# Optimization experiments

Measured on AMD Instinct MI355X. Metric: run time of the kernel, lower is better.

## Reference

```python
import jax, jax.numpy as jnp
import numpy as np

LABEL_SIZE = 64
START = LABEL_SIZE - 2
STOP = LABEL_SIZE - 1
NEG = -10000.0


def setup_inputs() -> dict:
    key = jax.random.key(0)
    k1, k2 = jax.random.split(key)
    B, T, L = 512, 512, LABEL_SIZE
    emissions = jax.random.normal(k1, (B, T, L), dtype=jnp.float32)
    # xavier-uniform-ish init, then mask row START (nothing transitions INTO start
    # ... actually transitions[next, prev]: row START = transitions into START)
    bound = float(np.sqrt(6.0 / (L + L)))
    trans = jax.random.uniform(k2, (L, L), dtype=jnp.float32, minval=-bound, maxval=bound)
    trans = trans.at[START, :].set(NEG)   # never transition to START
    trans = trans.at[:, STOP].set(NEG)    # never transition from STOP
    return {"input": emissions, "transitions": trans}


def reference(input, transitions):
    # input: [B, T, L] emission scores; transitions[next_tag, prev_tag]: [L, L]
    B, T, L = input.shape
    init = jnp.full((B, L), NEG, dtype=input.dtype).at[:, START].set(0.0)

    def step(forward_var, emit_t):
        # forward_var: [B, L] (over prev tag); emit_t: [B, L] (over next tag)
        # scores[b, next, prev] = forward_var[b, prev] + transitions[next, prev]
        nv = jax.nn.logsumexp(forward_var[:, None, :] + transitions[None, :, :], axis=-1)
        return nv + emit_t, None

    forward_var, _ = jax.lax.scan(step, init, jnp.swapaxes(input, 0, 1))  # scan over T
    terminal = forward_var + transitions[STOP][None, :]
    return jax.nn.logsumexp(terminal, axis=-1)  # [B] log partition function
```

## Files before the change

kernel.cpp:

```cpp
#include <hip/hip_runtime.h>

#define NTAG 64
#define TLEN 512
#define START_TAG 62
#define STOP_TAG 63
#define CHUNK 32
#define HALF (TLEN / 2)

__global__ __launch_bounds__(128) void crf_fwd_bwd(
    const float* __restrict__ emis,
    const float* __restrict__ trans,
    float* __restrict__ out)
{
    const int b    = blockIdx.x;
    const int tid  = threadIdx.x;
    const int lane = tid & 63;
    const int w    = tid >> 6;

    __shared__ float  lds[2 * 2 * CHUNK * NTAG];
    __shared__ float4 xb4[2][NTAG / 4];
    __shared__ float  sh[2][NTAG];

    const float L2E = 1.4426950408889634f;
    const float LN2 = 0.6931471805599453f;

    float E[NTAG];
    if (w == 0) {
        const float4* rowp = (const float4*)(trans + lane * NTAG);
        #pragma unroll
        for (int k4 = 0; k4 < NTAG / 4; ++k4) {
            float4 v = rowp[k4];
            E[4 * k4 + 0] = exp2f(v.x * L2E);
            E[4 * k4 + 1] = exp2f(v.y * L2E);
            E[4 * k4 + 2] = exp2f(v.z * L2E);
            E[4 * k4 + 3] = exp2f(v.w * L2E);
        }
    } else {
        #pragma unroll
        for (int k = 0; k < NTAG; ++k)
            E[k] = exp2f(trans[k * NTAG + lane] * L2E);
    }

    const float* eb = emis + (size_t)b * TLEN * NTAG;
    float* xbuf = (float*)xb4[w];

    float4 r0, r1, r2, r3, r4, r5, r6, r7;
    #define LOAD_CHUNK(baseT)                                        \
        do {                                                         \
            const float4* gp = (const float4*)(eb + (baseT) * NTAG); \
            r0 = gp[0 * 64 + lane]; r1 = gp[1 * 64 + lane];          \
            r2 = gp[2 * 64 + lane]; r3 = gp[3 * 64 + lane];          \
            r4 = gp[4 * 64 + lane]; r5 = gp[5 * 64 + lane];          \
            r6 = gp[6 * 64 + lane]; r7 = gp[7 * 64 + lane];          \
        } while (0)

    #define EXP4(v) make_float4(exp2f((v).x * L2E), exp2f((v).y * L2E), \
                                exp2f((v).z * L2E), exp2f((v).w * L2E))
    #define STORE_CHUNK_EXP(bufp)                                    \
        do {                                                         \
            float4* b4 = (float4*)(bufp);                            \
            b4[0 * 64 + lane] = EXP4(r0); b4[1 * 64 + lane] = EXP4(r1); \
            b4[2 * 64 + lane] = EXP4(r2); b4[3 * 64 + lane] = EXP4(r3); \
            b4[4 * 64 + lane] = EXP4(r4); b4[5 * 64 + lane] = EXP4(r5); \
            b4[6 * 64 + lane] = EXP4(r6); b4[7 * 64 + lane] = EXP4(r7); \
        } while (0)

    #define BMATVEC(ssum, xref)                                      \
        do {                                                         \
            const float4* xq_ = (const float4*)xbuf;                 \
            float4 xv_[16];                                          \
            _Pragma("unroll")                                        \
            for (int j = 0; j < 16; ++j) xv_[j] = xq_[j];            \
            xref = xv_[0].x;                                         \
            float a0=0.f,a1=0.f,a2=0.f,a3=0.f;                       \
            float a4=0.f,a5=0.f,a6=0.f,a7=0.f;                       \
            _Pragma("unroll")                                        \
            for (int j = 0; j < 16; j += 2) {                        \
                a0 = fmaf(xv_[j].x,     E[4*j + 0], a0);             \
                a1 = fmaf(xv_[j].y,     E[4*j + 1], a1);             \
                a2 = fmaf(xv_[j].z,     E[4*j + 2], a2);             \
                a3 = fmaf(xv_[j].w,     E[4*j + 3], a3);             \
                a4 = fmaf(xv_[j + 1].x, E[4*j + 4], a4);             \
                a5 = fmaf(xv_[j + 1].y, E[4*j + 5], a5);             \
                a6 = fmaf(xv_[j + 1].z, E[4*j + 6], a6);             \
                a7 = fmaf(xv_[j + 1].w, E[4*j + 7], a7);             \
            }                                                        \
            ssum = ((a0 + a1) + (a2 + a3)) + ((a4 + a5) + (a6 + a7)); \
        } while (0)

    #define RSCALE(xref, off, val)                                        \
        do {                                                              \
            int e_ = (int)((__float_as_uint(xref) >> 23) & 0xffu) - 127;  \
            off += e_;                                                    \
            val *= __uint_as_float((unsigned)(127 - e_) << 23);           \
        } while (0)

    float x;
    int   off = 0;

    if (w == 0) {
        x = (lane == START_TAG) ? 1.0f : 0.0f;
        xbuf[lane] = x;

        LOAD_CHUNK(0);
        #pragma clang loop unroll(disable)
        for (int ci = 0; ci < 8; ++ci) {
            float* buf = &lds[(ci & 1) * (CHUNK * NTAG)];
            STORE_CHUNK_EXP(buf);
            if (ci < 7) LOAD_CHUNK((ci + 1) * CHUNK);

            #pragma clang loop unroll(disable)
            for (int sg = 0; sg < 8; ++sg) {
                #pragma unroll
                for (int q = 0; q < 4; ++q) {
                    const int s = sg * 4 + q;
                    float em = buf[s * NTAG + lane];
                    float ssum, xref;
                    BMATVEC(ssum, xref);
                    float xnew = ssum * em;
                    if (q == 3) RSCALE(xref, off, xnew);
                    xbuf[lane] = xnew;
                    x = xnew;
                }
            }
        }
    } else {
        x = exp2f(trans[STOP_TAG * NTAG + lane] * L2E);

        LOAD_CHUNK(HALF + 7 * CHUNK);
        #pragma clang loop unroll(disable)
        for (int i = 0; i < 8; ++i) {
            const int ci = 7 - i;
            float* buf = &lds[(2 + (i & 1)) * (CHUNK * NTAG)];
            STORE_CHUNK_EXP(buf);
            if (i < 7) LOAD_CHUNK(HALF + (ci - 1) * CHUNK);

            float wcur = buf[(CHUNK - 1) * NTAG + lane];
            #pragma clang loop unroll(disable)
            for (int sg = 0; sg < 8; ++sg) {
                #pragma unroll
                for (int q = 0; q < 4; ++q) {
                    const int s  = CHUNK - 1 - (sg * 4 + q);
                    const int sn = (s > 0) ? s - 1 : 0;
                    float wnext = buf[sn * NTAG + lane];
                    xbuf[lane] = x * wcur;
                    float ssum, xref;
                    BMATVEC(ssum, xref);
                    float xnew = ssum;
                    if (q == 3) RSCALE(xref, off, xnew);
                    x = xnew;
                    wcur = wnext;
                }
            }
        }
    }

    sh[w][lane] = log2f(x) + (float)off;
    __syncthreads();

    if (w == 0) {
        float v = sh[0][lane] + sh[1][lane];
        float m = v;
        #pragma unroll
        for (int d = 1; d < 64; d <<= 1) m = fmaxf(m, __shfl_xor(m, d, 64));
        float e = exp2f(v - m);
        #pragma unroll
        for (int d = 1; d < 64; d <<= 1) e += __shfl_xor(e, d, 64);
        if (lane == 0) out[b] = LN2 * (m + log2f(e));
    }
}

extern "C" void kernel_launch(void* const* d_in, const int* in_sizes, int n_in,
                              void* d_out, int out_size, void* d_ws, size_t ws_size,
                              hipStream_t stream) {
    const float* emis  = (const float*)d_in[0];
    const float* trans = (const float*)d_in[1];
    float* out = (float*)d_out;
    (void)in_sizes; (void)n_in; (void)out_size; (void)d_ws; (void)ws_size;
    crf_fwd_bwd<<<512, 128, 0, stream>>>(emis, trans, out);
}
```

Baseline: 146.4 us.

## Use bf16 dot2 for CRF recurrence matvec with per-step rescaling

Stores the exponentiated transition matrix packed as bf16 pairs and the shared state vector as bf16, so each step's 64-term matvec uses fdot2 instructions and needs half as many LDS reads and register slots. Rescaling now runs every step instead of every fourth, and the backward pass folds the emission multiply into the step. Running the probabilities in bf16 reduces accuracy in the log-partition result, and the extra per-step rescale adds a little ALU work.

Measured after the change: 145.0 us. No clear change (-0.9%).

```diff
diff --git a/kernel.cpp b/kernel.cpp
--- a/kernel.cpp
+++ b/kernel.cpp
@@ -1,4 +1,5 @@
 #include <hip/hip_runtime.h>
+#include <hip/hip_bf16.h>
 
 #define NTAG 64
 #define TLEN 512
@@ -6,6 +7,22 @@
 #define STOP_TAG 63
 #define CHUNK 32
 #define HALF (TLEN / 2)
+
+#if __has_builtin(__builtin_amdgcn_fdot2_f32_bf16)
+#define USE_DOT2 1
+typedef __attribute__((ext_vector_type(2))) __bf16 bfv2;
+typedef __attribute__((ext_vector_type(8))) __bf16 bfv8;
+#endif
+
+__device__ __forceinline__ unsigned short f2bfu(float f) {
+    __hip_bfloat16 h = __float2bfloat16(f);
+    unsigned short u; __builtin_memcpy(&u, &h, 2); return u;
+}
+#ifdef USE_DOT2
+__device__ __forceinline__ __bf16 f2bf(float f) {
+    unsigned short u = f2bfu(f); __bf16 b; __builtin_memcpy(&b, &u, 2); return b;
+}
+#endif
 
 __global__ __launch_bounds__(128) void crf_fwd_bwd(
     const float* __restrict__ emis,
@@ -17,32 +34,43 @@
     const int lane = tid & 63;
     const int w    = tid >> 6;
 
-    __shared__ float  lds[2 * 2 * CHUNK * NTAG];
-    __shared__ float4 xb4[2][NTAG / 4];
-    __shared__ float  sh[2][NTAG];
+    __shared__ float lds[2 * 2 * CHUNK * NTAG];
+#ifdef USE_DOT2
+    __shared__ __align__(16) unsigned short xbf[2][NTAG];
+    unsigned short* xs = xbf[w];
+#else
+    __shared__ __align__(16) float xf32[2][NTAG];
+    float* xs = xf32[w];
+#endif
+    __shared__ float shv[2][NTAG];
 
     const float L2E = 1.4426950408889634f;
     const float LN2 = 0.6931471805599453f;
 
+#ifdef USE_DOT2
+    bfv2 Epk[NTAG / 2];
+    #pragma unroll
+    for (int k2 = 0; k2 < NTAG / 2; ++k2) {
+        float e0, e1;
+        if (w == 0) {
+            e0 = exp2f(trans[lane * NTAG + 2 * k2]     * L2E);
+            e1 = exp2f(trans[lane * NTAG + 2 * k2 + 1] * L2E);
+        } else {
+            e0 = exp2f(trans[(2 * k2) * NTAG + lane]     * L2E);
+            e1 = exp2f(trans[(2 * k2 + 1) * NTAG + lane] * L2E);
+        }
+        bfv2 p; p[0] = f2bf(e0); p[1] = f2bf(e1);
+        Epk[k2] = p;
+    }
+#else
     float E[NTAG];
-    if (w == 0) {
-        const float4* rowp = (const float4*)(trans + lane * NTAG);
-        #pragma unroll
-        for (int k4 = 0; k4 < NTAG / 4; ++k4) {
-            float4 v = rowp[k4];
-            E[4 * k4 + 0] = exp2f(v.x * L2E);
-            E[4 * k4 + 1] = exp2f(v.y * L2E);
-            E[4 * k4 + 2] = exp2f(v.z * L2E);
-            E[4 * k4 + 3] = exp2f(v.w * L2E);
-        }
-    } else {
-        #pragma unroll
-        for (int k = 0; k < NTAG; ++k)
-            E[k] = exp2f(trans[k * NTAG + lane] * L2E);
-    }
+    #pragma unroll
+    for (int k = 0; k < NTAG; ++k)
+        E[k] = exp2f(((w == 0) ? trans[lane * NTAG + k]
+                               : trans[k * NTAG + lane]) * L2E);
+#endif
 
     const float* eb = emis + (size_t)b * TLEN * NTAG;
-    float* xbuf = (float*)xb4[w];
 
     float4 r0, r1, r2, r3, r4, r5, r6, r7;
     #define LOAD_CHUNK(baseT)                                        \
@@ -53,7 +81,6 @@
             r4 = gp[4 * 64 + lane]; r5 = gp[5 * 64 + lane];          \
             r6 = gp[6 * 64 + lane]; r7 = gp[7 * 64 + lane];          \
         } while (0)
-
     #define EXP4(v) make_float4(exp2f((v).x * L2E), exp2f((v).y * L2E), \
                                 exp2f((v).z * L2E), exp2f((v).w * L2E))
     #define STORE_CHUNK_EXP(bufp)                                    \
@@ -65,13 +92,39 @@
             b4[6 * 64 + lane] = EXP4(r6); b4[7 * 64 + lane] = EXP4(r7); \
         } while (0)
 
-    #define BMATVEC(ssum, xref)                                      \
-        do {                                                         \
-            const float4* xq_ = (const float4*)xbuf;                 \
+#ifdef USE_DOT2
+    #define PAIR(X, i) __builtin_shufflevector(X, X, 2 * (i), 2 * (i) + 1)
+    #define DOTQ(acc, X, base)                                                     \
+        acc = __builtin_amdgcn_fdot2_f32_bf16(Epk[(base) + 0], PAIR(X, 0), acc, false); \
+        acc = __builtin_amdgcn_fdot2_f32_bf16(Epk[(base) + 1], PAIR(X, 1), acc, false); \
+        acc = __builtin_amdgcn_fdot2_f32_bf16(Epk[(base) + 2], PAIR(X, 2), acc, false); \
+        acc = __builtin_amdgcn_fdot2_f32_bf16(Epk[(base) + 3], PAIR(X, 3), acc, false);
+    #define MATVEC_REF(ssum, e_)                                     \
+        do {                                                         \
+            const bfv8* xq_ = (const bfv8*)xs;                       \
+            bfv8 X0 = xq_[0], X1 = xq_[1], X2 = xq_[2], X3 = xq_[3]; \
+            bfv8 X4 = xq_[4], X5 = xq_[5], X6 = xq_[6], X7 = xq_[7]; \
+            unsigned short ru_;                                      \
+            { __bf16 rb_ = X0[0]; __builtin_memcpy(&ru_, &rb_, 2); } \
+            int ef_ = (int)((ru_ >> 7) & 0xffu);                     \
+            e_ = (ef_ == 0) ? 0 : ef_ - 127;                         \
+            float a0 = 0.f, a1 = 0.f, a2 = 0.f, a3 = 0.f;            \
+            DOTQ(a0, X0, 0)  DOTQ(a1, X1, 4)                         \
+            DOTQ(a2, X2, 8)  DOTQ(a3, X3, 12)                        \
+            DOTQ(a0, X4, 16) DOTQ(a1, X5, 20)                        \
+            DOTQ(a2, X6, 24) DOTQ(a3, X7, 28)                        \
+            ssum = (a0 + a1) + (a2 + a3);                            \
+        } while (0)
+    #define WRITE_STATE(v) (xs[lane] = f2bfu(v))
+#else
+    #define MATVEC_REF(ssum, e_)                                     \
+        do {                                                         \
+            const float4* xq_ = (const float4*)xs;                   \
             float4 xv_[16];                                          \
             _Pragma("unroll")                                        \
             for (int j = 0; j < 16; ++j) xv_[j] = xq_[j];            \
-            xref = xv_[0].x;                                         \
+            int ef_ = (int)((__float_as_uint(xv_[0].x) >> 23) & 0xffu); \
+            e_ = (ef_ == 0) ? 0 : ef_ - 127;                         \
             float a0=0.f,a1=0.f,a2=0.f,a3=0.f;                       \
             float a4=0.f,a5=0.f,a6=0.f,a7=0.f;                       \
             _Pragma("unroll")                                        \
@@ -87,20 +140,25 @@
             }                                                        \
             ssum = ((a0 + a1) + (a2 + a3)) + ((a4 + a5) + (a6 + a7)); \
         } while (0)
-
-    #define RSCALE(xref, off, val)                                        \
-        do {                                                              \
-            int e_ = (int)((__float_as_uint(xref) >> 23) & 0xffu) - 127;  \
-            off += e_;                                                    \
-            val *= __uint_as_float((unsigned)(127 - e_) << 23);           \
-        } while (0)
-
-    float x;
+    #define WRITE_STATE(v) (xs[lane] = (v))
+#endif
+
+    #define STEP(buf, s)                                             \
+        do {                                                         \
+            float em_ = (buf)[(s) * NTAG + lane];                    \
+            float ssum_; int e_;                                     \
+            MATVEC_REF(ssum_, e_);                                   \
+            off += e_;                                               \
+            float rs_ = __uint_as_float((unsigned)(127 - e_) << 23); \
+            x = ssum_ * em_ * rs_;                                   \
+            WRITE_STATE(x);                                          \
+        } while (0)
+
+    float x = 0.0f;
     int   off = 0;
 
     if (w == 0) {
-        x = (lane == START_TAG) ? 1.0f : 0.0f;
-        xbuf[lane] = x;
+        WRITE_STATE(lane == START_TAG ? 1.0f : 0.0f);
 
         LOAD_CHUNK(0);
         #pragma clang loop unroll(disable)
@@ -109,57 +167,40 @@
             STORE_CHUNK_EXP(buf);
             if (ci < 7) LOAD_CHUNK((ci + 1) * CHUNK);
 
-            #pragma clang loop unroll(disable)
-            for (int sg = 0; sg < 8; ++sg) {
-                #pragma unroll
-                for (int q = 0; q < 4; ++q) {
-                    const int s = sg * 4 + q;
-                    float em = buf[s * NTAG + lane];
-                    float ssum, xref;
-                    BMATVEC(ssum, xref);
-                    float xnew = ssum * em;
-                    if (q == 3) RSCALE(xref, off, xnew);
-                    xbuf[lane] = xnew;
-                    x = xnew;
-                }
-            }
+            #pragma clang loop unroll_count(4)
+            for (int s = 0; s < CHUNK; ++s) STEP(buf, s);
         }
     } else {
-        x = exp2f(trans[STOP_TAG * NTAG + lane] * L2E);
+        float Sv = exp2f(trans[STOP_TAG * NTAG + lane] * L2E);
 
         LOAD_CHUNK(HALF + 7 * CHUNK);
         #pragma clang loop unroll(disable)
         for (int i = 0; i < 8; ++i) {
-            const int ci = 7 - i;
             float* buf = &lds[(2 + (i & 1)) * (CHUNK * NTAG)];
             STORE_CHUNK_EXP(buf);
-            if (i < 7) LOAD_CHUNK(HALF + (ci - 1) * CHUNK);
-
-            float wcur = buf[(CHUNK - 1) * NTAG + lane];
-            #pragma clang loop unroll(disable)
-            for (int sg = 0; sg < 8; ++sg) {
-                #pragma unroll
-                for (int q = 0; q < 4; ++q) {
-                    const int s  = CHUNK - 1 - (sg * 4 + q);
-                    const int sn = (s > 0) ? s - 1 : 0;
-                    float wnext = buf[sn * NTAG + lane];
-                    xbuf[lane] = x * wcur;
-                    float ssum, xref;
-                    BMATVEC(ssum, xref);
-                    float xnew = ssum;
-                    if (q == 3) RSCALE(xref, off, xnew);
-                    x = xnew;
-                    wcur = wnext;
-                }
+            if (i < 7) LOAD_CHUNK(HALF + (6 - i) * CHUNK);
+
+            int s0 = CHUNK - 1;
+            if (i == 0) {
+                WRITE_STATE(Sv * buf[(CHUNK - 1) * NTAG + lane]);
+                s0 = CHUNK - 2;
             }
+            #pragma clang loop unroll_count(4)
+            for (int s = s0; s >= 0; --s) STEP(buf, s);
+        }
+        {
+            float ssum_; int e_;
+            MATVEC_REF(ssum_, e_);
+            off += e_;
+            x = ssum_ * __uint_as_float((unsigned)(127 - e_) << 23);
         }
     }
 
-    sh[w][lane] = log2f(x) + (float)off;
+    shv[w][lane] = log2f(x) + (float)off;
     __syncthreads();
 
     if (w == 0) {
-        float v = sh[0][lane] + sh[1][lane];
+        float v = shv[0][lane] + shv[1][lane];
         float m = v;
         #pragma unroll
         for (int d = 1; d < 64; d <<= 1) m = fmaxf(m, __shfl_xor(m, d, 64));
```
